# Performance work log

Hardware: AMD Instinct MI355X
Metric: run time of the kernel (lower is better)

Reference implementation:

```python
import jax, jax.numpy as jnp
import numpy as np

EMBED_DIM = 512
NUM_HEADS = 8
GLOBAL_MIX = 0.5


def setup_inputs() -> dict:
    key = jax.random.key(0)
    ks = jax.random.split(key, 7)
    B, L, E = 8, 1024, EMBED_DIM
    s = 1.0 / np.sqrt(E)
    x = jax.random.normal(ks[0], (B, L, E), dtype=jnp.float32)
    mask = jax.random.randint(ks[1], (B, L), 0, 2) > 0  # True = valid token
    Wq = jax.random.normal(ks[2], (E, E), dtype=jnp.float32) * s
    Wk = jax.random.normal(ks[3], (E, E), dtype=jnp.float32) * s
    Wv = jax.random.normal(ks[4], (E, E), dtype=jnp.float32) * s
    Wo = jax.random.normal(ks[5], (E, E), dtype=jnp.float32) * s
    G = jax.random.normal(ks[6], (L, L), dtype=jnp.float32)
    return {"x": x, "mask": mask, "Wq": Wq, "Wk": Wk, "Wv": Wv, "Wo": Wo, "G": G}


def _tanh_mha(x, mask, Wq, Wk, Wv, Wo, G):
    B, L, E = x.shape
    H = NUM_HEADS
    D = E // H
    scale = 1.0 / np.sqrt(D)
    dt = x.dtype
    fmax = jnp.finfo(dt).max
    tiny = jnp.finfo(dt).tiny

    def split_heads(t):  # (B,L,E) -> (B,H,L,D)
        return t.reshape(B, L, H, D).transpose(0, 2, 1, 3)

    q = split_heads(x @ Wq.T)
    k = split_heads(x @ Wk.T)
    v = split_heads(x @ Wv.T)

    scores = jnp.tanh(jnp.einsum('bhqd,bhkd->bhqk', q, k) * scale)
    key_valid = mask[:, None, None, :]  # (B,1,1,L)
    scores = jnp.where(key_valid, scores, -jnp.inf)

    finite = jnp.isfinite(scores)
    finite_scores = jnp.where(finite, scores, -fmax)
    m = jnp.max(finite_scores, axis=(1, 2, 3), keepdims=True)  # per-sample amax over heads+q+k
    m = jnp.where(jnp.isfinite(m), m, jnp.zeros_like(m))
    exp_scores = jnp.where(finite, jnp.exp(scores - m), jnp.zeros_like(scores))

    mf = mask.astype(dt)
    exp_scores = exp_scores * mf[:, None, None, :] * mf[:, None, :, None]
    denom = jnp.maximum(exp_scores.sum(axis=(1, 2, 3), keepdims=True), tiny)
    weights = exp_scores / denom
    # dropout p=0 -> identity; renorm pass kept for faithfulness
    renorm = jnp.maximum(weights.sum(axis=(1, 2, 3), keepdims=True), tiny)
    weights = weights / renorm

    # learnable global attention: softmax rows, clamp, mask, normalize over (q,k)
    activated = jnp.maximum(jax.nn.softmax(G, axis=-1), 0.0)  # (L,L)
    gscores = activated[None] * mf[:, None, :] * mf[:, :, None]  # (B,L,L)
    gsums = jnp.maximum(gscores.sum(axis=(1, 2), keepdims=True), tiny)
    gnorm = (gscores / gsums)[:, None]  # (B,1,L,L)
    weights = (1.0 - GLOBAL_MIX) * weights + GLOBAL_MIX * gnorm

    attended = jnp.einsum('bhqk,bhkd->bhqd', weights, v)
    attended = attended * mf[:, None, :, None]
    attended = attended.transpose(0, 2, 1, 3).reshape(B, L, E)
    return attended @ Wo.T


def reference(x, mask, Wq, Wk, Wv, Wo, G):
    return _tanh_mha(x, mask, Wq, Wk, Wv, Wo, G)
```

## Files before the change

### kernel.cpp

```cpp
#include <hip/hip_runtime.h>
#include <math.h>

#define B_ 8
#define L_ 1024
#define E_ 512
#define H_ 8
#define D_ 64
#define QSZ (B_*H_*L_*D_)
#define BLE ((size_t)B_*L_*E_)
#define TINYF 1.175494350822287508e-38f
#define SWK(r) ((((r) ^ ((r) >> 3))) & 7)

typedef unsigned short u16;
typedef __attribute__((ext_vector_type(8))) short bfrag;
typedef __attribute__((ext_vector_type(4))) float ffrag;
typedef __attribute__((ext_vector_type(16))) float ffrag16;
typedef __attribute__((ext_vector_type(4))) short vshort4;

#if __has_builtin(__builtin_amdgcn_exp2f)
#define EXP2F(x) __builtin_amdgcn_exp2f(x)
#else
#define EXP2F(x) __expf((x) * 0.6931471805599453f)
#endif
#if __has_builtin(__builtin_amdgcn_rcpf)
#define RCPF(x) __builtin_amdgcn_rcpf(x)
#else
#define RCPF(x) (1.0f / (x))
#endif

__device__ __forceinline__ u16 f2b(float f) {
  unsigned u = __float_as_uint(f);
  u += 0x7fffu + ((u >> 16) & 1u);
  return (u16)(u >> 16);
}
__device__ __forceinline__ unsigned pk2(float a, float b) {
  unsigned ua = __float_as_uint(a); ua += 0x7fffu + ((ua >> 16) & 1u);
  unsigned ub = __float_as_uint(b); ub += 0x7fffu + ((ub >> 16) & 1u);
  return (ua >> 16) | (ub & 0xffff0000u);
}
__device__ __forceinline__ float blo(unsigned u) { return __uint_as_float(u << 16); }
__device__ __forceinline__ float bhi(unsigned u) { return __uint_as_float(u & 0xffff0000u); }

__device__ __forceinline__ bfrag cvt8v(const float* __restrict__ src) {
  float4 a = *(const float4*)src;
  float4 b = *(const float4*)(src + 4);
  bfrag r;
  r[0]=(short)f2b(a.x); r[1]=(short)f2b(a.y); r[2]=(short)f2b(a.z); r[3]=(short)f2b(a.w);
  r[4]=(short)f2b(b.x); r[5]=(short)f2b(b.y); r[6]=(short)f2b(b.z); r[7]=(short)f2b(b.w);
  return r;
}

__device__ __forceinline__ void gll16(const void* g, void* l) {
  __builtin_amdgcn_global_load_lds(
      (const __attribute__((address_space(1))) void*)g,
      (__attribute__((address_space(3))) void*)l, 16, 0, 0);
}

__global__ __launch_bounds__(256) void prep_softmax_k(
    const float* __restrict__ x, const float* __restrict__ Wq,
    const float* __restrict__ Wk, const float* __restrict__ Wv,
    const float* __restrict__ Wo, const float* __restrict__ G,
    const int* __restrict__ mask,
    u16* __restrict__ xb, u16* __restrict__ Wb, u16* __restrict__ actb,
    float* __restrict__ R) {
  const int bid = blockIdx.x, t = threadIdx.x;
  __shared__ float sred[8];
  __shared__ float rred[4][8];
  if (bid < 2048) {
    size_t c = (size_t)bid * 256 + t;
    *(bfrag*)&xb[c * 8] = cvt8v(x + c * 8);
    return;
  }
  if (bid < 2560) {
    const int c2 = bid - 2048;
    const float* src = (c2 < 128) ? Wq : (c2 < 256) ? Wk : (c2 < 384) ? Wv : Wo;
    const size_t base = (size_t)(c2 >> 7) * 262144;
    const size_t cc = (size_t)(c2 & 127) * 256 + t;
    *(bfrag*)&Wb[base + cc * 8] = cvt8v(src + cc * 8);
    return;
  }
  const int q = bid - 2560;
  const int w = t >> 6, lane = t & 63;
  float4 g4 = ((const float4*)(G + (size_t)q * 1024))[t];
  float m = fmaxf(fmaxf(g4.x, g4.y), fmaxf(g4.z, g4.w));
#pragma unroll
  for (int off = 32; off > 0; off >>= 1) m = fmaxf(m, __shfl_down(m, off));
  if (lane == 0) sred[w] = m;
  __syncthreads();
  m = fmaxf(fmaxf(sred[0], sred[1]), fmaxf(sred[2], sred[3]));
  float e0 = __expf(g4.x - m), e1 = __expf(g4.y - m);
  float e2 = __expf(g4.z - m), e3 = __expf(g4.w - m);
  float s = e0 + e1 + e2 + e3;
#pragma unroll
  for (int off = 32; off > 0; off >>= 1) s += __shfl_down(s, off);
  if (lane == 0) sred[4 + w] = s;
  __syncthreads();
  const float inv = 1.0f / (sred[4] + sred[5] + sred[6] + sred[7]);
  const unsigned p0 = pk2(e0 * inv, e1 * inv);
  const unsigned p1 = pk2(e2 * inv, e3 * inv);
  *(uint2*)&actb[(size_t)q * 1024 + t * 4] = make_uint2(p0, p1);
  const float r0 = blo(p0), r1 = bhi(p0);
  const float r2 = blo(p1), r3 = bhi(p1);
  float rd[8];
#pragma unroll
  for (int b = 0; b < 8; ++b) {
    const int* mkp = mask + b * 1024 + t * 4;
    rd[b] = (mkp[0] ? r0 : 0.f) + (mkp[1] ? r1 : 0.f) +
            (mkp[2] ? r2 : 0.f) + (mkp[3] ? r3 : 0.f);
#pragma unroll
    for (int off = 32; off > 0; off >>= 1) rd[b] += __shfl_down(rd[b], off);
  }
  if (lane == 0)
#pragma unroll
    for (int b = 0; b < 8; ++b) rred[w][b] = rd[b];
  __syncthreads();
  if (t < 8) R[q * 8 + t] = rred[0][t] + rred[1][t] + rred[2][t] + rred[3][t];
}

__global__ __launch_bounds__(256) void proj_k(
    const u16* __restrict__ xb, const u16* __restrict__ Wb,
    const int* __restrict__ mask, const float* __restrict__ R,
    float* __restrict__ sums,
    u16* __restrict__ Qb, u16* __restrict__ Kb, u16* __restrict__ Vtb) {
  const int m0 = blockIdx.x * 128;
  const int n0 = blockIdx.y * 128;
  __shared__ __align__(16) u16 As[128 * 64];
  __shared__ __align__(16) u16 Bs[128 * 64];
  __shared__ float rr[4][8];
  const int t = threadIdx.x, w = t >> 6, lane = t & 63;
  const int l15 = lane & 15, quad = lane >> 4;
  const int mq = (w >> 1) * 64, nq = (w & 1) * 64;

  if (blockIdx.x == 0 && blockIdx.y == 0) {
    float a8[8] = {0,0,0,0,0,0,0,0};
    for (int q = t; q < 1024; q += 256)
#pragma unroll
      for (int b = 0; b < 8; ++b)
        if (mask[b * 1024 + q]) a8[b] += R[q * 8 + b];
#pragma unroll
    for (int b = 0; b < 8; ++b) {
#pragma unroll
      for (int off = 32; off > 0; off >>= 1) a8[b] += __shfl_down(a8[b], off);
    }
    if (lane == 0)
#pragma unroll
      for (int b = 0; b < 8; ++b) rr[w][b] = a8[b];
    __syncthreads();
    if (t < 8) {
      sums[t] = 0.0f;
      sums[8 + t] = rr[0][t] + rr[1][t] + rr[2][t] + rr[3][t];
    }
  }

  const ffrag fz = {0.f, 0.f, 0.f, 0.f};
  ffrag acc[4][4];
#pragma unroll
  for (int i = 0; i < 4; ++i)
#pragma unroll
    for (int j = 0; j < 4; ++j) acc[i][j] = fz;

  for (int kk = 0; kk < 512; kk += 64) {
    __syncthreads();
#pragma unroll
    for (int j = 0; j < 4; ++j) {
      const int c = w * 256 + j * 64 + lane;
      const int row = c >> 3, ck = (c & 7) ^ (row & 7);
      gll16(xb + (size_t)(m0 + row) * 512 + kk + ck * 8,
            &As[(size_t)(w * 256 + j * 64) * 8]);
    }
#pragma unroll
    for (int j = 0; j < 4; ++j) {
      const int c = w * 256 + j * 64 + lane;
      const int row = c >> 3, ck = (c & 7) ^ (row & 7);
      gll16(Wb + (size_t)(n0 + row) * 512 + kk + ck * 8,
            &Bs[(size_t)(w * 256 + j * 64) * 8]);
    }
    __syncthreads();
#pragma unroll
    for (int s = 0; s < 2; ++s) {
      bfrag av[4], bv[4];
#pragma unroll
      for (int i = 0; i < 4; ++i) {
        const int ar = mq + i * 16 + l15;
        av[i] = *(const bfrag*)&As[ar * 64 + (((quad + 4 * s) ^ (ar & 7)) << 3)];
        const int br = nq + i * 16 + l15;
        bv[i] = *(const bfrag*)&Bs[br * 64 + (((quad + 4 * s) ^ (br & 7)) << 3)];
      }
#pragma unroll
      for (int i = 0; i < 4; ++i)
#pragma unroll
        for (int j = 0; j < 4; ++j)
          acc[i][j] = __builtin_amdgcn_mfma_f32_16x16x32_bf16(av[i], bv[j], acc[i][j], 0, 0, 0);
    }
  }
  const int z = n0 >> 9;
  const int c0 = n0 & 511;
#pragma unroll
  for (int i = 0; i < 4; ++i) {
    const int mbase = m0 + mq + i * 16 + quad * 4;
    const int b = mbase >> 10, l0 = mbase & 1023;
#pragma unroll
    for (int j = 0; j < 4; ++j) {
      const int nc = c0 + nq + j * 16 + l15;
      const int h = nc >> 6, d = nc & 63;
      if (z == 0) {
        u16* dst = Qb + ((size_t)(b * 8 + h) * 1024 + l0) * 64 + d;
#pragma unroll
        for (int r = 0; r < 4; ++r) dst[(size_t)r * 64] = f2b(acc[i][j][r]);
      } else if (z == 1) {
        u16* dst = Kb + ((size_t)(b * 8 + h) * 1024 + l0) * 64 + d;
#pragma unroll
        for (int r = 0; r < 4; ++r) dst[(size_t)r * 64] = f2b(acc[i][j][r]);
      } else {
        vshort4 vs;
#pragma unroll
        for (int r = 0; r < 4; ++r)
          vs[r] = (short)(mask[b * 1024 + l0 + r] ? f2b(acc[i][j][r]) : (u16)0);
        *(vshort4*)(Vtb + ((size_t)(b * 8 + h) * 64 + d) * 1024 + l0) = vs;
      }
    }
  }
}

__global__ __launch_bounds__(256) void attn_gv_k(
    const u16* __restrict__ Qb, const u16* __restrict__ Kb,
    const u16* __restrict__ Vtb, const u16* __restrict__ actb,
    const int* __restrict__ mask,
    u16* __restrict__ AEb, u16* __restrict__ AGb, float* __restrict__ denom) {
  __shared__ __align__(16) u16 POOL[13320];
  const int t = threadIdx.x, w = t >> 6, lane = t & 63;
  const int l15 = lane & 15, quad = lane >> 4;

  if (blockIdx.x < 512) {
    u16* As = POOL;
    u16* Bs = POOL + 4096;
    const int mt = blockIdx.x & 127, nt = blockIdx.x >> 7;
    const int m0 = mt * 64, n0 = nt * 128;
    const int b = mt >> 4;
    const int q0 = (mt & 15) * 64;
    const int mq = (w >> 1) * 32, nq = (w & 1) * 64;
    const ffrag fz = {0.f, 0.f, 0.f, 0.f};
    ffrag acc[2][4];
#pragma unroll
    for (int i = 0; i < 2; ++i)
#pragma unroll
      for (int j = 0; j < 4; ++j) acc[i][j] = fz;

    for (int kk = 0; kk < 1024; kk += 64) {
      __syncthreads();
#pragma unroll
      for (int j = 0; j < 2; ++j) {
        const int c = w * 128 + j * 64 + lane;
        const int row = c >> 3, ck = (c & 7) ^ (row & 7);
        gll16(actb + (size_t)(q0 + row) * 1024 + kk + ck * 8,
              &As[(size_t)(w * 128 + j * 64) * 8]);
      }
#pragma unroll
      for (int j = 0; j < 4; ++j) {
        const int c = w * 256 + j * 64 + lane;
        const int row = c >> 3, ck = (c & 7) ^ (row & 7);
        gll16(Vtb + (size_t)(b * 512 + n0 + row) * 1024 + kk + ck * 8,
              &Bs[(size_t)(w * 256 + j * 64) * 8]);
      }
      __syncthreads();
#pragma unroll
      for (int s = 0; s < 2; ++s) {
        bfrag av[2], bv[4];
#pragma unroll
        for (int i = 0; i < 2; ++i) {
          const int ar = mq + i * 16 + l15;
          av[i] = *(const bfrag*)&As[ar * 64 + (((quad + 4 * s) ^ (ar & 7)) << 3)];
        }
#pragma unroll
        for (int j = 0; j < 4; ++j) {
          const int br = nq + j * 16 + l15;
          bv[j] = *(const bfrag*)&Bs[br * 64 + (((quad + 4 * s) ^ (br & 7)) << 3)];
        }
#pragma unroll
        for (int i = 0; i < 2; ++i)
#pragma unroll
          for (int j = 0; j < 4; ++j)
            acc[i][j] = __builtin_amdgcn_mfma_f32_16x16x32_bf16(av[i], bv[j], acc[i][j], 0, 0, 0);
      }
    }
#pragma unroll
    for (int i = 0; i < 2; ++i) {
      const int mbase = m0 + mq + i * 16 + quad * 4;
#pragma unroll
      for (int j = 0; j < 4; ++j) {
        const int n = n0 + nq + j * 16 + l15;
#pragma unroll
        for (int r = 0; r < 4; ++r)
          AGb[(size_t)(mbase + r) * 512 + n] = f2b(acc[i][j][r]);
      }
    }
    return;
  }

  const int aid = blockIdx.x - 512;
  const int qt = aid & 15;
  const int bh = aid >> 4;
  const int b = bh >> 3, h = bh & 7;
  u16* Ks = POOL;
  u16* Vs = POOL + 4096;
  u16* Es = POOL + 8192;
  u16* Ms = POOL + 12288;
  float* red4 = (float*)(POOL + 13312);
  const int l31 = lane & 31, hi = lane >> 5;
  const int qsb = w >> 1, msb = w & 1;
  const int qpb = w & 1, dpb = w >> 1;

  const u16* Kg = Kb + (size_t)bh * 65536;
  const u16* Vg = Vtb + (size_t)bh * 65536;

  const u16* Qrow = Qb + ((size_t)bh * 1024 + qt * 64 + qsb * 32 + l31) * 64;
  bfrag qf[4];
#pragma unroll
  for (int ko = 0; ko < 4; ++ko) qf[ko] = *(const bfrag*)(Qrow + ko * 16 + hi * 8);

  {
    int4 mi = *(const int4*)(mask + b * 1024 + t * 4);
    vshort4 mv;
    mv[0] = mi.x ? (short)0x3F80 : (short)0; mv[1] = mi.y ? (short)0x3F80 : (short)0;
    mv[2] = mi.z ? (short)0x3F80 : (short)0; mv[3] = mi.w ? (short)0x3F80 : (short)0;
    *(vshort4*)&Ms[t * 4] = mv;
  }

  auto stageK = [&](int kt) {
#pragma unroll
    for (int j = 0; j < 2; ++j) {
      const int c = w * 128 + j * 64 + lane;
      const int row = c >> 3, ck = (c & 7) ^ SWK(row);
      gll16(Kg + (size_t)(kt * 64 + row) * 64 + ck * 8,
            &Ks[(size_t)(w * 128 + j * 64) * 8]);
    }
  };
  auto stageV = [&](int kt) {
#pragma unroll
    for (int j = 0; j < 2; ++j) {
      const int c = w * 128 + j * 64 + lane;
      const int row = c >> 3, ck = (c & 7) ^ SWK(row);
      gll16(Vg + (size_t)row * 1024 + kt * 64 + ck * 8,
            &Vs[(size_t)(w * 128 + j * 64) * 8]);
    }
  };

  stageK(0); stageV(0);
  __syncthreads();

  ffrag16 accE, dacc;
#pragma unroll
  for (int i = 0; i < 16; ++i) { accE[i] = 0.f; dacc[i] = 0.f; }

  for (int kt = 0; kt < 16; ++kt) {
    ffrag16 st;
#pragma unroll
    for (int i = 0; i < 16; ++i) st[i] = 0.f;
    const int krow = msb * 32 + l31;
    const int kk7 = SWK(krow);
#pragma unroll
    for (int ko = 0; ko < 4; ++ko) {
      bfrag ak = *(const bfrag*)&Ks[krow * 64 + (((ko * 2 + hi) ^ kk7) << 3)];
      st = __builtin_amdgcn_mfma_f32_32x32x16_bf16(ak, qf[ko], st, 0, 0, 0);
    }
    const int qrow = qsb * 32 + l31;
    const int qk7 = SWK(qrow);
#pragma unroll
    for (int g = 0; g < 4; ++g) {
      float ee[4];
#pragma unroll
      for (int r = 0; r < 4; ++r) {
        const float tt = EXP2F(st[4 * g + r] * 0.360673760222f);
        ee[r] = EXP2F(RCPF(tt + 1.0f) * -2.88539008178f);
      }
      const int k0 = msb * 32 + g * 8 + hi * 4;
      *(uint2*)&Es[qrow * 64 + (((k0 >> 3) ^ qk7) << 3) + (k0 & 7)] =
          make_uint2(pk2(ee[0], ee[1]), pk2(ee[2], ee[3]));
    }
    __syncthreads();
    if (kt < 15) stageK(kt + 1);

    const int erow = qpb * 32 + l31;
    const int ek7 = SWK(erow);
    const int vrow = dpb * 32 + l31;
    const int vk7 = SWK(vrow);
#pragma unroll
    for (int ko = 0; ko < 4; ++ko) {
      const int co = ko * 2 + hi;
      bfrag ea = *(const bfrag*)&Es[erow * 64 + ((co ^ ek7) << 3)];
      bfrag bv = *(const bfrag*)&Vs[vrow * 64 + ((co ^ vk7) << 3)];
      accE = __builtin_amdgcn_mfma_f32_32x32x16_bf16(ea, bv, accE, 0, 0, 0);
      if (dpb == 0) {
        bfrag bm = *(const bfrag*)&Ms[kt * 64 + ko * 16 + hi * 8];
        dacc = __builtin_amdgcn_mfma_f32_32x32x16_bf16(ea, bm, dacc, 0, 0, 0);
      }
    }
    __syncthreads();
    if (kt < 15) stageV(kt + 1);
  }

  const size_t obase = ((size_t)(b * 1024 + qt * 64 + qpb * 32)) * 512
                       + h * 64 + dpb * 32 + l31;
#pragma unroll
  for (int r = 0; r < 16; ++r) {
    const int qloc = (r & 3) + 8 * (r >> 2) + 4 * hi;
    AEb[obase + (size_t)qloc * 512] = f2b(accE[r]);
  }
  float dsumv = 0.0f;
  if (l31 == 0 && dpb == 0) {
    const int qb0 = b * 1024 + qt * 64 + qpb * 32 + 4 * hi;
#pragma unroll
    for (int r = 0; r < 16; ++r) {
      const int q = qb0 + (r & 3) + 8 * (r >> 2);
      dsumv += mask[q] ? dacc[r] : 0.0f;
    }
    red4[qpb * 2 + hi] = dsumv;
  }
  __syncthreads();
  if (t == 0) atomicAdd(denom + b, red4[0] + red4[1] + red4[2] + red4[3]);
}

__global__ __launch_bounds__(256) void o_proj_k(
    const u16* __restrict__ AEb, const u16* __restrict__ AGb,
    const int* __restrict__ mask, const float* __restrict__ sums,
    const u16* __restrict__ Wb, float* __restrict__ out) {
  const int m0 = blockIdx.x * 128;
  const int n0 = blockIdx.y * 128;
  const int b = m0 >> 10;
  const float c1 = 0.5f / fmaxf(sums[b], TINYF);
  const float c2 = 0.5f / fmaxf(sums[8 + b], TINYF);
  __shared__ __align__(16) u16 As[128 * 64];
  __shared__ __align__(16) u16 Bs[128 * 64];
  const int t = threadIdx.x, w = t >> 6, lane = t & 63;
  const int l15 = lane & 15, quad = lane >> 4;
  const int mq = (w >> 1) * 64, nq = (w & 1) * 64;
  int rowi[4]; float c1r[4], c2r[4];
#pragma unroll
  for (int i = 0; i < 4; ++i) {
    const int c = t + i * 256;
    rowi[i] = c >> 3;
    const int mqv = mask[b * 1024 + ((m0 + rowi[i]) & 1023)];
    c1r[i] = mqv ? c1 : 0.0f;
    c2r[i] = mqv ? c2 : 0.0f;
  }
  const ffrag fz = {0.f, 0.f, 0.f, 0.f};
  ffrag acc[4][4];
#pragma unroll
  for (int i = 0; i < 4; ++i)
#pragma unroll
    for (int j = 0; j < 4; ++j) acc[i][j] = fz;

  for (int kk = 0; kk < 512; kk += 64) {
    __syncthreads();
#pragma unroll
    for (int i = 0; i < 4; ++i) {
      const int c = t + i * 256;
      const int row = rowi[i], ck = c & 7;
      const size_t gofs = (size_t)(m0 + row) * 512 + kk + ck * 8;
      uint4 ua = *(const uint4*)(AEb + gofs);
      uint4 ug = *(const uint4*)(AGb + gofs);
      const float a1 = c1r[i], a2 = c2r[i];
      uint4 res;
      res.x = pk2(a1 * blo(ua.x) + a2 * blo(ug.x), a1 * bhi(ua.x) + a2 * bhi(ug.x));
      res.y = pk2(a1 * blo(ua.y) + a2 * blo(ug.y), a1 * bhi(ua.y) + a2 * bhi(ug.y));
      res.z = pk2(a1 * blo(ua.z) + a2 * blo(ug.z), a1 * bhi(ua.z) + a2 * bhi(ug.z));
      res.w = pk2(a1 * blo(ua.w) + a2 * blo(ug.w), a1 * bhi(ua.w) + a2 * bhi(ug.w));
      *(uint4*)&As[row * 64 + ((ck ^ (row & 7)) << 3)] = res;
    }
#pragma unroll
    for (int j = 0; j < 4; ++j) {
      const int c = w * 256 + j * 64 + lane;
      const int row = c >> 3, ck = (c & 7) ^ (row & 7);
      gll16(Wb + (size_t)(1536 + n0 + row) * 512 + kk + ck * 8,
            &Bs[(size_t)(w * 256 + j * 64) * 8]);
    }
    __syncthreads();
#pragma unroll
    for (int s = 0; s < 2; ++s) {
      bfrag av[4], bv[4];
#pragma unroll
      for (int i = 0; i < 4; ++i) {
        const int ar = mq + i * 16 + l15;
        av[i] = *(const bfrag*)&As[ar * 64 + (((quad + 4 * s) ^ (ar & 7)) << 3)];
        const int br = nq + i * 16 + l15;
        bv[i] = *(const bfrag*)&Bs[br * 64 + (((quad + 4 * s) ^ (br & 7)) << 3)];
      }
#pragma unroll
      for (int i = 0; i < 4; ++i)
#pragma unroll
        for (int j = 0; j < 4; ++j)
          acc[i][j] = __builtin_amdgcn_mfma_f32_16x16x32_bf16(av[i], bv[j], acc[i][j], 0, 0, 0);
    }
  }
#pragma unroll
  for (int i = 0; i < 4; ++i) {
    const int mbase = m0 + mq + i * 16 + quad * 4;
#pragma unroll
    for (int j = 0; j < 4; ++j) {
      const int n = n0 + nq + j * 16 + l15;
#pragma unroll
      for (int r = 0; r < 4; ++r)
        out[(size_t)(mbase + r) * 512 + n] = acc[i][j][r];
    }
  }
}

extern "C" void kernel_launch(void* const* d_in, const int* in_sizes, int n_in,
                              void* d_out, int out_size, void* d_ws, size_t ws_size,
                              hipStream_t stream) {
  const float* x  = (const float*)d_in[0];
  const int* mask = (const int*)d_in[1];
  const float* Wq = (const float*)d_in[2];
  const float* Wk = (const float*)d_in[3];
  const float* Wv = (const float*)d_in[4];
  const float* Wo = (const float*)d_in[5];
  const float* G  = (const float*)d_in[6];
  float* out = (float*)d_out;

  u16* xb   = (u16*)d_ws;
  u16* Wb   = xb + (size_t)8192 * 512;
  u16* Qb   = Wb + (size_t)2048 * 512;
  u16* Kb   = Qb + QSZ;
  u16* Vtb  = Kb + QSZ;
  u16* actb = Vtb + QSZ;
  u16* AEb  = actb + (size_t)1024 * 1024;
  u16* AGb  = AEb + BLE;
  float* R  = (float*)(AGb + BLE);
  float* SUMS = R + 8192;

  prep_softmax_k<<<3584, 256, 0, stream>>>(x, Wq, Wk, Wv, Wo, G, mask, xb, Wb, actb, R);
  proj_k<<<dim3(64, 12), 256, 0, stream>>>(xb, Wb, mask, R, SUMS, Qb, Kb, Vtb);
  attn_gv_k<<<1536, 256, 0, stream>>>(Qb, Kb, Vtb, actb, mask, AEb, AGb, SUMS);
  o_proj_k<<<dim3(64, 4), 256, 0, stream>>>(AEb, AGb, mask, SUMS, Wb, out);
}
```

Measured before the change: 183.8 us.

## Compact valid query rows and skip attention tiles beyond valid count

Adds a per-batch prefix scan of the mask that maps each token to a compacted position, with valid tokens first, plus a count of valid tokens. Q rows are scattered to those positions so attention blocks whose query tile lies entirely past the valid count exit early. The output projection gathers AE rows through the same map and zeros masked rows. About half the query tiles are skipped for a random mask, at the cost of scattered Q writes and an extra indirection in o_proj.

```diff
diff --git a/kernel.cpp b/kernel.cpp
--- a/kernel.cpp
+++ b/kernel.cpp
@@ -62,10 +62,11 @@
     const float* __restrict__ Wo, const float* __restrict__ G,
     const int* __restrict__ mask,
     u16* __restrict__ xb, u16* __restrict__ Wb, u16* __restrict__ actb,
-    float* __restrict__ R) {
+    float* __restrict__ R, int* __restrict__ posb, int* __restrict__ nvb) {
   const int bid = blockIdx.x, t = threadIdx.x;
   __shared__ float sred[8];
   __shared__ float rred[4][8];
+  __shared__ int sc[256];
   if (bid < 2048) {
     size_t c = (size_t)bid * 256 + t;
     *(bfrag*)&xb[c * 8] = cvt8v(x + c * 8);
@@ -77,6 +78,33 @@
     const size_t base = (size_t)(c2 >> 7) * 262144;
     const size_t cc = (size_t)(c2 & 127) * 256 + t;
     *(bfrag*)&Wb[base + cc * 8] = cvt8v(src + cc * 8);
+    return;
+  }
+  if (bid >= 3584) {
+    const int bb = bid - 3584;
+    int4 mi = *(const int4*)(mask + bb * 1024 + t * 4);
+    const int vx = mi.x ? 1 : 0, vy = mi.y ? 1 : 0;
+    const int vz = mi.z ? 1 : 0, vw = mi.w ? 1 : 0;
+    const int c0 = vx + vy + vz + vw;
+    sc[t] = c0;
+    __syncthreads();
+#pragma unroll
+    for (int off = 1; off < 256; off <<= 1) {
+      int v = (t >= off) ? sc[t - off] : 0;
+      __syncthreads();
+      sc[t] += v;
+      __syncthreads();
+    }
+    const int nvtot = sc[255];
+    int pv = sc[t] - c0;
+    int pi = t * 4 - pv;
+    int4 pq;
+    pq.x = vx ? pv : nvtot + pi; pv += vx; pi += 1 - vx;
+    pq.y = vy ? pv : nvtot + pi; pv += vy; pi += 1 - vy;
+    pq.z = vz ? pv : nvtot + pi; pv += vz; pi += 1 - vz;
+    pq.w = vw ? pv : nvtot + pi;
+    *(int4*)(posb + bb * 1024 + t * 4) = pq;
+    if (t == 0) nvb[bb] = nvtot;
     return;
   }
   const int q = bid - 2560;
@@ -120,6 +148,7 @@
 __global__ __launch_bounds__(256) void proj_k(
     const u16* __restrict__ xb, const u16* __restrict__ Wb,
     const int* __restrict__ mask, const float* __restrict__ R,
+    const int* __restrict__ posb,
     float* __restrict__ sums,
     u16* __restrict__ Qb, u16* __restrict__ Kb, u16* __restrict__ Vtb) {
   const int m0 = blockIdx.x * 128;
@@ -199,14 +228,18 @@
   for (int i = 0; i < 4; ++i) {
     const int mbase = m0 + mq + i * 16 + quad * 4;
     const int b = mbase >> 10, l0 = mbase & 1023;
+    int4 pr;
+    if (z == 0) pr = *(const int4*)(posb + b * 1024 + l0);
 #pragma unroll
     for (int j = 0; j < 4; ++j) {
       const int nc = c0 + nq + j * 16 + l15;
       const int h = nc >> 6, d = nc & 63;
       if (z == 0) {
-        u16* dst = Qb + ((size_t)(b * 8 + h) * 1024 + l0) * 64 + d;
-#pragma unroll
-        for (int r = 0; r < 4; ++r) dst[(size_t)r * 64] = f2b(acc[i][j][r]);
+        u16* dst = Qb + (size_t)(b * 8 + h) * 65536 + d;
+        dst[(size_t)pr.x * 64] = f2b(acc[i][j][0]);
+        dst[(size_t)pr.y * 64] = f2b(acc[i][j][1]);
+        dst[(size_t)pr.z * 64] = f2b(acc[i][j][2]);
+        dst[(size_t)pr.w * 64] = f2b(acc[i][j][3]);
       } else if (z == 1) {
         u16* dst = Kb + ((size_t)(b * 8 + h) * 1024 + l0) * 64 + d;
 #pragma unroll
@@ -225,7 +258,7 @@
 __global__ __launch_bounds__(256) void attn_gv_k(
     const u16* __restrict__ Qb, const u16* __restrict__ Kb,
     const u16* __restrict__ Vtb, const u16* __restrict__ actb,
-    const int* __restrict__ mask,
+    const int* __restrict__ mask, const int* __restrict__ nvb,
     u16* __restrict__ AEb, u16* __restrict__ AGb, float* __restrict__ denom) {
   __shared__ __align__(16) u16 POOL[13320];
   const int t = threadIdx.x, w = t >> 6, lane = t & 63;
@@ -301,6 +334,8 @@
   const int qt = aid & 15;
   const int bh = aid >> 4;
   const int b = bh >> 3, h = bh & 7;
+  const int nv = nvb[b];
+  if (qt * 64 >= nv) return;
   u16* Ks = POOL;
   u16* Vs = POOL + 4096;
   u16* Es = POOL + 8192;
@@ -408,11 +443,11 @@
   }
   float dsumv = 0.0f;
   if (l31 == 0 && dpb == 0) {
-    const int qb0 = b * 1024 + qt * 64 + qpb * 32 + 4 * hi;
+    const int cq0 = qt * 64 + qpb * 32 + 4 * hi;
 #pragma unroll
     for (int r = 0; r < 16; ++r) {
-      const int q = qb0 + (r & 3) + 8 * (r >> 2);
-      dsumv += mask[q] ? dacc[r] : 0.0f;
+      const int cq = cq0 + (r & 3) + 8 * (r >> 2);
+      dsumv += (cq < nv) ? dacc[r] : 0.0f;
     }
     red4[qpb * 2 + hi] = dsumv;
   }
@@ -422,7 +457,8 @@
 
 __global__ __launch_bounds__(256) void o_proj_k(
     const u16* __restrict__ AEb, const u16* __restrict__ AGb,
-    const int* __restrict__ mask, const float* __restrict__ sums,
+    const int* __restrict__ mask, const int* __restrict__ posb,
+    const float* __restrict__ sums,
     const u16* __restrict__ Wb, float* __restrict__ out) {
   const int m0 = blockIdx.x * 128;
   const int n0 = blockIdx.y * 128;
@@ -434,14 +470,16 @@
   const int t = threadIdx.x, w = t >> 6, lane = t & 63;
   const int l15 = lane & 15, quad = lane >> 4;
   const int mq = (w >> 1) * 64, nq = (w & 1) * 64;
-  int rowi[4]; float c1r[4], c2r[4];
+  int rowi[4], prw[4], mrow[4]; float c1r[4], c2r[4];
 #pragma unroll
   for (int i = 0; i < 4; ++i) {
     const int c = t + i * 256;
     rowi[i] = c >> 3;
-    const int mqv = mask[b * 1024 + ((m0 + rowi[i]) & 1023)];
-    c1r[i] = mqv ? c1 : 0.0f;
-    c2r[i] = mqv ? c2 : 0.0f;
+    const int tok = (m0 + rowi[i]) & 1023;
+    mrow[i] = mask[b * 1024 + tok];
+    prw[i] = posb[b * 1024 + tok];
+    c1r[i] = mrow[i] ? c1 : 0.0f;
+    c2r[i] = mrow[i] ? c2 : 0.0f;
   }
   const ffrag fz = {0.f, 0.f, 0.f, 0.f};
   ffrag acc[4][4];
@@ -457,7 +495,9 @@
       const int c = t + i * 256;
       const int row = rowi[i], ck = c & 7;
       const size_t gofs = (size_t)(m0 + row) * 512 + kk + ck * 8;
-      uint4 ua = *(const uint4*)(AEb + gofs);
+      const size_t gofsE = (size_t)(b * 1024 + prw[i]) * 512 + kk + ck * 8;
+      uint4 ua = *(const uint4*)(AEb + gofsE);
+      if (!mrow[i]) ua = make_uint4(0u, 0u, 0u, 0u);
       uint4 ug = *(const uint4*)(AGb + gofs);
       const float a1 = c1r[i], a2 = c2r[i];
       uint4 res;
@@ -527,9 +567,11 @@
   u16* AGb  = AEb + BLE;
   float* R  = (float*)(AGb + BLE);
   float* SUMS = R + 8192;
-
-  prep_softmax_k<<<3584, 256, 0, stream>>>(x, Wq, Wk, Wv, Wo, G, mask, xb, Wb, actb, R);
-  proj_k<<<dim3(64, 12), 256, 0, stream>>>(xb, Wb, mask, R, SUMS, Qb, Kb, Vtb);
-  attn_gv_k<<<1536, 256, 0, stream>>>(Qb, Kb, Vtb, actb, mask, AEb, AGb, SUMS);
-  o_proj_k<<<dim3(64, 4), 256, 0, stream>>>(AEb, AGb, mask, SUMS, Wb, out);
-}
+  int* posb = (int*)(SUMS + 16);
+  int* nvb  = posb + 8192;
+
+  prep_softmax_k<<<3592, 256, 0, stream>>>(x, Wq, Wk, Wv, Wo, G, mask, xb, Wb, actb, R, posb, nvb);
+  proj_k<<<dim3(64, 12), 256, 0, stream>>>(xb, Wb, mask, R, posb, SUMS, Qb, Kb, Vtb);
+  attn_gv_k<<<1536, 256, 0, stream>>>(Qb, Kb, Vtb, actb, mask, nvb, AEb, AGb, SUMS);
+  o_proj_k<<<dim3(64, 4), 256, 0, stream>>>(AEb, AGb, mask, posb, SUMS, Wb, out);
+}
```

Result: no change. 183.7 us (-0.1%).
